# Optimization experiments

Measured on AMD Instinct MI355X. Metric: run time of the kernel, lower is better.

## Reference

```python
import jax, jax.numpy as jnp
import numpy as np

EPS = 0.0001
N_NODES = 8192
N_GRAPHS = 128
NODES_PER_G = 64
N_FEAT = 128
CLDIM = 512
LAYERS = 3
HEADS = 8
HID = 64
N_EDGES = 262144
N_CLASSES = 10


def setup_inputs():
    key = jax.random.key(0)
    ks = jax.random.split(key, 12)
    x = jax.random.normal(ks[0], (N_NODES, N_FEAT), jnp.float32)

    def rand_edges(k):
        k1, k2 = jax.random.split(k)
        g = jax.random.randint(k1, (N_EDGES,), 0, N_GRAPHS)
        loc = jax.random.randint(k2, (2, N_EDGES), 0, NODES_PER_G)
        return (g[None, :] * NODES_PER_G + loc).astype(jnp.int32)

    edge_index = rand_edges(ks[1])
    neg_edge_index = rand_edges(ks[2])
    batch = (jnp.arange(N_NODES) // NODES_PER_G).astype(jnp.int32)
    # mask indices: all within-graph node pairs (block-diagonal mask==1)
    base = jnp.arange(N_GRAPHS) * NODES_PER_G
    a = jnp.repeat(jnp.arange(NODES_PER_G), NODES_PER_G)
    b = jnp.tile(jnp.arange(NODES_PER_G), NODES_PER_G)
    midx = jnp.stack([
        (base[:, None] + a[None, :]).reshape(-1),
        (base[:, None] + b[None, :]).reshape(-1),
    ]).astype(jnp.int32)
    s = 0.05
    return dict(
        x=x, edge_index=edge_index, neg_edge_index=neg_edge_index,
        batch=batch, midx=midx,
        fc_W=jax.random.normal(ks[3], (N_FEAT, CLDIM), jnp.float32) * s,
        fc_b=jnp.zeros((CLDIM,), jnp.float32),
        bn_g=jnp.ones((LAYERS, CLDIM), jnp.float32),
        bn_b=jnp.zeros((LAYERS, CLDIM), jnp.float32),
        conv_W=jax.random.normal(ks[4], (LAYERS, CLDIM, CLDIM), jnp.float32) * s,
        conv_b=jnp.zeros((LAYERS, CLDIM), jnp.float32),
        feat_W=jax.random.normal(ks[5], (LAYERS * CLDIM, HEADS * HID), jnp.float32) * s,
        phi=jax.random.normal(ks[6], (HEADS, 2 * HID, 1), jnp.float32) * s,
        fc1_W=jax.random.normal(ks[7], (HEADS * HID, HID), jnp.float32) * s,
        fc1_b=jnp.zeros((HID,), jnp.float32),
        fc2_W=jax.random.normal(ks[8], (HID, N_CLASSES), jnp.float32) * s,
        fc2_b=jnp.zeros((N_CLASSES,), jnp.float32),
    )


def _bn(h, g, b):
    # BatchNorm1d in training mode (biased variance over nodes)
    m = jnp.mean(h, 0)
    v = jnp.var(h, 0)
    return (h - m) * jax.lax.rsqrt(v + 1e-5) * g + b


def _gcn(h, W, b, src, dst, n):
    # GCNConv with added self-loops: D^-1/2 (A+I) D^-1/2 (h W) + b
    h2 = h @ W
    deg = jax.ops.segment_sum(jnp.ones(src.shape[0], h.dtype), dst, n) + 1.0
    dinv = jax.lax.rsqrt(deg)
    coef = (dinv[src] * dinv[dst])[:, None]
    agg = jax.ops.segment_sum(h2[src] * coef, dst, n)
    return agg + h2 / deg[:, None] + b


def _forward(x, fc_W, fc_b, bn_g, bn_b, conv_W, conv_b, feat_W, phi,
             fc1_W, fc1_b, fc2_W, fc2_b, edge_index, neg_edge_index, batch, midx):
    n = x.shape[0]
    h = x @ fc_W + fc_b
    src, dst = edge_index[0], edge_index[1]
    hs = []
    for i in range(LAYERS):
        h = _bn(h, bn_g[i], bn_b[i])
        h = jax.nn.relu(_gcn(h, conv_W[i], conv_b[i], src, dst, n))
        hs.append(h)
    z = jnp.concatenate(hs, -1)  # [N, LAYERS*CLDIM]

    # ---- recon loss: per-edge inner-product decoder, mean-pooled per graph ----
    def edge_loss(ei, neg):
        v = jnp.sum(z[ei[0]] * z[ei[1]], -1)
        sgm = jax.nn.sigmoid(v)
        l = -jnp.log(EPS + (1.0 - sgm if neg else sgm))
        seg = batch[ei[0]]
        cnt = jax.ops.segment_sum(jnp.ones_like(l), seg, N_GRAPHS)
        tot = jax.ops.segment_sum(l, seg, N_GRAPHS)
        return jnp.sum(tot / jnp.maximum(cnt, 1.0))

    Lrc = (edge_loss(edge_index, False) + edge_loss(neg_edge_index, True)) / N_GRAPHS

    # ---- classifier: multi-head sigmoid attention over mask pairs ----
    xh = (z @ feat_W).reshape(n, HEADS, HID)
    phi_a = phi[:, :HID, 0]   # [H, HID]
    phi_b = phi[:, HID:, 0]   # [H, HID]
    # cat([x_i, x_j]) @ phi == x_i @ phi_a + x_j @ phi_b, computed per node then gathered
    s1 = jnp.einsum('nhd,hd->nh', xh, phi_a)
    s2 = jnp.einsum('nhd,hd->nh', xh, phi_b)
    w = jax.nn.sigmoid(jax.nn.leaky_relu(s1[midx[0]] + s2[midx[1]]))  # [M, H]
    msg = (xh[midx[1]] * w[:, :, None]).reshape(-1, HEADS * HID)      # [M, H*HID]
    agg = jax.ops.segment_sum(msg, midx[0], n)
    logits = jax.nn.leaky_relu(agg @ fc1_W + fc1_b) @ fc2_W + fc2_b
    tmp = jnp.exp(logits - jnp.max(logits, -1, keepdims=True)) + EPS
    preds = tmp / jnp.sum(tmp, -1, keepdims=True)
    cnt = jax.ops.segment_sum(jnp.ones((n,), preds.dtype), batch, N_GRAPHS)
    yp = jax.ops.segment_sum(preds, batch, N_GRAPHS) / cnt[:, None]
    return jnp.log(yp), Lrc, preds


def reference(x, edge_index, neg_edge_index, batch, midx, fc_W, fc_b, bn_g, bn_b,
              conv_W, conv_b, feat_W, phi, fc1_W, fc1_b, fc2_W, fc2_b):
    return _forward(x, fc_W, fc_b, bn_g, bn_b, conv_W, conv_b, feat_W, phi,
                    fc1_W, fc1_b, fc2_W, fc2_b, edge_index, neg_edge_index, batch, midx)
```

## Files before the change

### kernel.cpp

```cpp
#include <hip/hip_runtime.h>

#define NN 8192
#define NG 128
#define NF 128
#define CL 512
#define ZD 1536
#define NE 262144

typedef __attribute__((ext_vector_type(8))) _Float16 half8;
typedef __attribute__((ext_vector_type(4))) float f32x4;

__global__ void deg_kernel(const int* __restrict__ dst, float* __restrict__ deg) {
    int e = blockIdx.x * 256 + threadIdx.x;
    atomicAdd(&deg[dst[e]], 1.0f);
}

__global__ void build_adj(const int* __restrict__ src, const int* __restrict__ dst,
                          const float* __restrict__ deg, float* __restrict__ A) {
    int e = blockIdx.x * 256 + threadIdx.x;
    int s = src[e], d = dst[e];
    int g = d >> 6;
    float w = rsqrtf(deg[s] + 1.0f) * rsqrtf(deg[d] + 1.0f);
    atomicAdd(&A[(size_t)((g << 6) + (d & 63)) * 64 + (s & 63)], w);
}

__global__ void cvtA(const float* __restrict__ Amat, const float* __restrict__ deg,
                     _Float16* __restrict__ Ah) {
    int t = blockIdx.x * 256 + threadIdx.x;
    int i4 = t * 4;
    int g = i4 >> 12, loc = i4 & 4095;
    float4 v = *(const float4*)(Amat + (size_t)g * 4096 + loc);
    float vv[4] = {v.x, v.y, v.z, v.w};
    int row = loc >> 6;
    int c0 = loc & 63;
    int ed = row - c0;
    if (ed >= 0 && ed < 4) vv[ed] += 1.0f / (deg[g * 64 + row] + 1.0f);
    int swz = (row & 7) << 3;
    #pragma unroll
    for (int e = 0; e < 4; ++e)
        Ah[(size_t)g * 4096 + ((loc + e) ^ swz)] = (_Float16)vv[e];
}

__global__ void cvt_h(const float* __restrict__ in, _Float16* __restrict__ out) {
    int i = blockIdx.x * 256 + threadIdx.x;
    float4 a = *(const float4*)(in + (size_t)i * 8);
    float4 b = *(const float4*)(in + (size_t)i * 8 + 4);
    half8 o;
    o[0] = (_Float16)a.x; o[1] = (_Float16)a.y; o[2] = (_Float16)a.z; o[3] = (_Float16)a.w;
    o[4] = (_Float16)b.x; o[5] = (_Float16)b.y; o[6] = (_Float16)b.z; o[7] = (_Float16)b.w;
    *(half8*)(out + (size_t)i * 8) = o;
}

__global__ void cvtT(const float* __restrict__ W, _Float16* __restrict__ Wt,
                     int Kd, int Nd) {
    __shared__ float t[32][33];
    int kb = blockIdx.y * 32, nb = blockIdx.x * 32;
    int tx = threadIdx.x, ty = threadIdx.y;
    for (int i = ty; i < 32; i += 8)
        t[i][tx] = W[(size_t)(kb + i) * Nd + nb + tx];
    __syncthreads();
    for (int i = ty; i < 32; i += 8)
        Wt[(size_t)(nb + i) * Kd + kb + tx] = (_Float16)t[tx][i];
}

__global__ void wprep(const float* __restrict__ W,
                      const float* __restrict__ sums, const float* __restrict__ sqs,
                      const float* __restrict__ g, const float* __restrict__ b,
                      _Float16* __restrict__ Wt, float* __restrict__ bias2,
                      int Kd, int Nd) {
    __shared__ float t[32][33];
    __shared__ float tks[32];
    int kb = blockIdx.y * 32, nb = blockIdx.x * 32;
    int tx = threadIdx.x, ty = threadIdx.y;
    for (int i = ty; i < 32; i += 8)
        t[i][tx] = W[(size_t)(kb + i) * Nd + nb + tx];
    int kc = kb + tx;
    float m = sums[kc] * (1.0f / NN);
    float var = sqs[kc] * (1.0f / NN) - m * m;
    float sc = rsqrtf(var + 1e-5f) * g[kc];
    if (ty == 0) tks[tx] = b[kc] - m * sc;
    __syncthreads();
    for (int i = ty; i < 32; i += 8)
        Wt[(size_t)(nb + i) * Kd + kb + tx] = (_Float16)(t[tx][i] * sc);
    if (ty == 0) {
        float acc = 0.f;
        #pragma unroll
        for (int i = 0; i < 32; ++i) acc = fmaf(tks[i], t[i][tx], acc);
        atomicAdd(&bias2[nb + tx], acc);
    }
}

template<int ACT, bool HASB, bool OUT16, bool STATS, bool FUSE>
__global__ __launch_bounds__(256)
void gemm_f16(const _Float16* __restrict__ A, int lda,
              const _Float16* __restrict__ Bt, int ldb,
              float* __restrict__ Cf, _Float16* __restrict__ Ch, int ldc,
              const float* __restrict__ bias, int K,
              float* __restrict__ sums, float* __restrict__ sqs,
              const _Float16* __restrict__ Ahg,
              const float* __restrict__ cb,
              _Float16* __restrict__ Zout)
{
    __shared__ __align__(16) char SMraw[FUSE ? 34816 : 24576];
    _Float16* As = (_Float16*)SMraw;
    _Float16* Bs = (_Float16*)(SMraw + 16384);
    const int tid = threadIdx.x;
    const int lane = tid & 63, wave = tid >> 6;
    const int wr = wave >> 1, wc = wave & 1;
    const int ntile = gridDim.x;
    const int li = blockIdx.y * ntile + blockIdx.x;
    const int x8 = li & 7, rest = li >> 3;
    const int bt = rest % ntile;
    const int bp = (rest / ntile) * 8 + x8;
    const int bm = bp * 128, bn = bt * 64;

    f32x4 acc[4][2];
    #pragma unroll
    for (int m = 0; m < 4; ++m)
        #pragma unroll
        for (int n = 0; n < 2; ++n)
            acc[m][n] = (f32x4){0.f, 0.f, 0.f, 0.f};

    const int fl = lane & 15, kh = (lane >> 4) * 8;
    const int sw = (fl & 7) << 3;

    for (int k0 = 0; k0 < K; k0 += 64) {
        #pragma unroll
        for (int j = 0; j < 4; ++j) {
            int d = wave * 2048 + j * 512 + lane * 8;
            int row = d >> 6, kk = d & 63;
            int sk = kk ^ ((row & 7) << 3);
            __builtin_amdgcn_global_load_lds(
                (const __attribute__((address_space(1))) void*)(A + (size_t)(bm + row) * lda + k0 + sk),
                (__attribute__((address_space(3))) void*)&As[wave * 2048 + j * 512], 16, 0, 0);
        }
        #pragma unroll
        for (int j = 0; j < 2; ++j) {
            int d = wave * 1024 + j * 512 + lane * 8;
            int row = d >> 6, kk = d & 63;
            int sk = kk ^ ((row & 7) << 3);
            __builtin_amdgcn_global_load_lds(
                (const __attribute__((address_space(1))) void*)(Bt + (size_t)(bn + row) * ldb + k0 + sk),
                (__attribute__((address_space(3))) void*)&Bs[wave * 1024 + j * 512], 16, 0, 0);
        }
        __syncthreads();
        #pragma unroll
        for (int kc = 0; kc < 2; ++kc) {
            int ko = (kc * 32 + kh) ^ sw;
            half8 av[4], bv[2];
            #pragma unroll
            for (int m = 0; m < 4; ++m)
                av[m] = *(const half8*)&As[(wr * 64 + m * 16 + fl) * 64 + ko];
            #pragma unroll
            for (int n = 0; n < 2; ++n)
                bv[n] = *(const half8*)&Bs[(wc * 32 + n * 16 + fl) * 64 + ko];
            #pragma unroll
            for (int m = 0; m < 4; ++m)
                #pragma unroll
                for (int n = 0; n < 2; ++n)
                    acc[m][n] = __builtin_amdgcn_mfma_f32_16x16x32_f16(av[m], bv[n], acc[m][n], 0, 0, 0);
        }
        __syncthreads();
    }

    const int orow0 = (lane >> 4) * 4;
    const int ocol  = lane & 15;

    if constexpr (!FUSE) {
        #pragma unroll
        for (int n = 0; n < 2; ++n) {
            int col = bn + wc * 32 + n * 16 + ocol;
            float bb = HASB ? bias[col] : 0.f;
            float ss = 0.f, qq = 0.f;
            #pragma unroll
            for (int m = 0; m < 4; ++m) {
                #pragma unroll
                for (int r = 0; r < 4; ++r) {
                    int rowg = bm + wr * 64 + m * 16 + orow0 + r;
                    float v = acc[m][n][r] + bb;
                    if (ACT == 2) v = v > 0.f ? v : 0.01f * v;
                    if (STATS) { ss += v; qq = fmaf(v, v, qq); }
                    if (OUT16) Ch[(size_t)rowg * ldc + col] = (_Float16)v;
                    else       Cf[(size_t)rowg * ldc + col] = v;
                }
            }
            if (STATS) {
                ss += __shfl_down(ss, 32); ss += __shfl_down(ss, 16);
                qq += __shfl_down(qq, 32); qq += __shfl_down(qq, 16);
                if (lane < 16) {
                    atomicAdd(&sums[col], ss);
                    atomicAdd(&sqs[col], qq);
                }
            }
        }
    } else {
        _Float16* AsA = (_Float16*)SMraw;
        _Float16* Xs  = (_Float16*)(SMraw + 16384);
        const _Float16* Ag = Ahg + (size_t)(bm >> 6) * 4096;
        #pragma unroll
        for (int j = 0; j < 4; ++j)
            __builtin_amdgcn_global_load_lds(
                (const __attribute__((address_space(1))) void*)(Ag + wave * 2048 + j * 512 + lane * 8),
                (__attribute__((address_space(3))) void*)&AsA[wave * 2048 + j * 512], 16, 0, 0);
        #pragma unroll
        for (int n = 0; n < 2; ++n) {
            int c = wc * 32 + n * 16 + ocol;
            float bb = HASB ? bias[bn + c] : 0.f;
            int csw = (c & 7) << 3;
            #pragma unroll
            for (int m = 0; m < 4; ++m) {
                #pragma unroll
                for (int r = 0; r < 4; ++r) {
                    int srow = wr * 64 + m * 16 + orow0 + r;
                    Xs[c * 128 + (srow & 64) + ((srow & 63) ^ csw)] = (_Float16)(acc[m][n][r] + bb);
                }
            }
        }
        __syncthreads();
        const int gg = wave >> 1, rh = wave & 1;
        f32x4 acc2[2][4];
        #pragma unroll
        for (int m2 = 0; m2 < 2; ++m2)
            #pragma unroll
            for (int n2 = 0; n2 < 4; ++n2)
                acc2[m2][n2] = (f32x4){0.f, 0.f, 0.f, 0.f};
        #pragma unroll
        for (int kc = 0; kc < 2; ++kc) {
            int ko = (kc * 32 + kh) ^ sw;
            #pragma unroll
            for (int m2 = 0; m2 < 2; ++m2) {
                int arow = rh * 32 + m2 * 16 + fl;
                half8 av = *(const half8*)&AsA[gg * 4096 + arow * 64 + ko];
                #pragma unroll
                for (int n2 = 0; n2 < 4; ++n2) {
                    int c = n2 * 16 + fl;
                    half8 bv = *(const half8*)&Xs[c * 128 + gg * 64 + ((kc * 32 + kh) ^ ((c & 7) << 3))];
                    acc2[m2][n2] = __builtin_amdgcn_mfma_f32_16x16x32_f16(av, bv, acc2[m2][n2], 0, 0, 0);
                }
            }
        }
        __syncthreads();
        float* Cs = (float*)SMraw;
        #pragma unroll
        for (int m2 = 0; m2 < 2; ++m2)
            #pragma unroll
            for (int n2 = 0; n2 < 4; ++n2)
                #pragma unroll
                for (int r = 0; r < 4; ++r)
                    Cs[(gg * 64 + rh * 32 + m2 * 16 + orow0 + r) * 68 + n2 * 16 + ocol] = acc2[m2][n2][r];
        __syncthreads();
        const int rr = tid >> 3, dq = tid & 7;
        #pragma unroll
        for (int pass = 0; pass < 4; ++pass) {
            int row = pass * 32 + rr;
            half8 hv;
            #pragma unroll
            for (int e = 0; e < 8; ++e) {
                float v = Cs[row * 68 + dq * 8 + e] + cb[bn + dq * 8 + e];
                v = v > 0.f ? v : 0.f;
                hv[e] = (_Float16)v;
            }
            *(half8*)(Zout + (size_t)(bm + row) * ZD + bn + dq * 8) = hv;
        }
        if (STATS && tid < 64) {
            float bb = cb[bn + tid];
            float ss = 0.f, qq = 0.f;
            for (int row = 0; row < 128; ++row) {
                float v = Cs[row * 68 + tid] + bb;
                v = v > 0.f ? v : 0.f;
                ss += v;
                qq = fmaf(v, v, qq);
            }
            atomicAdd(&sums[bn + tid], ss);
            atomicAdd(&sqs[bn + tid], qq);
        }
    }
}

__global__ __launch_bounds__(256)
void gram_mfma(const _Float16* __restrict__ Z, float* __restrict__ Gparts)
{
    __shared__ _Float16 Zs[4096];
    const int g = blockIdx.x, khalf = blockIdx.y;
    const int tid = threadIdx.x;
    const int lane = tid & 63, wave = tid >> 6;
    const int fl = lane & 15, kh = (lane >> 4) * 8;
    const int sw = (fl & 7) << 3;
    float* G = Gparts + (size_t)khalf * NG * 4096;

    f32x4 acc[4];
    #pragma unroll
    for (int n = 0; n < 4; ++n) acc[n] = (f32x4){0.f, 0.f, 0.f, 0.f};

    for (int k0 = khalf * (ZD / 2); k0 < (khalf + 1) * (ZD / 2); k0 += 64) {
        #pragma unroll
        for (int j = 0; j < 2; ++j) {
            int d = wave * 1024 + j * 512 + lane * 8;
            int row = d >> 6, kk = d & 63;
            int sk = kk ^ ((row & 7) << 3);
            __builtin_amdgcn_global_load_lds(
                (const __attribute__((address_space(1))) void*)(Z + (size_t)(g * 64 + row) * ZD + k0 + sk),
                (__attribute__((address_space(3))) void*)&Zs[wave * 1024 + j * 512], 16, 0, 0);
        }
        __syncthreads();
        #pragma unroll
        for (int kc = 0; kc < 2; ++kc) {
            int ko = (kc * 32 + kh) ^ sw;
            half8 av = *(const half8*)&Zs[(wave * 16 + fl) * 64 + ko];
            #pragma unroll
            for (int n = 0; n < 4; ++n) {
                half8 bv = *(const half8*)&Zs[(n * 16 + fl) * 64 + ko];
                acc[n] = __builtin_amdgcn_mfma_f32_16x16x32_f16(av, bv, acc[n], 0, 0, 0);
            }
        }
        __syncthreads();
    }
    const int orow0 = (lane >> 4) * 4;
    const int ocol  = lane & 15;
    #pragma unroll
    for (int n = 0; n < 4; ++n)
        #pragma unroll
        for (int r = 0; r < 4; ++r)
            G[(size_t)(g * 64 + wave * 16 + orow0 + r) * 64 + n * 16 + ocol] = acc[n][r];
}

__global__ void edge_loss2(const int* __restrict__ ei, const int* __restrict__ nei,
                           const float* __restrict__ G0, float* __restrict__ LOSS)
{
    const int setid = blockIdx.y;
    const int* e0 = setid ? nei : ei;
    const int* e1 = e0 + NE;
    float* tot = LOSS + setid * 256;
    float* cnt = tot + 128;
    const float* G1 = G0 + (size_t)NG * 4096;
    __shared__ float lt[128];
    __shared__ float lc[128];
    int tid = threadIdx.x;
    if (tid < 128) { lt[tid] = 0.f; lc[tid] = 0.f; }
    __syncthreads();
    for (int e = blockIdx.x * blockDim.x + tid; e < NE; e += gridDim.x * blockDim.x) {
        int a = e0[e], b = e1[e];
        int g = a >> 6;
        size_t idx = (size_t)((g << 6) + (a & 63)) * 64 + (b & 63);
        float v = G0[idx] + G1[idx];
        float s = 1.f / (1.f + expf(-v));
        float p = setid ? (1.f - s) : s;
        float l = -logf(1e-4f + p);
        atomicAdd(&lt[g], l);
        atomicAdd(&lc[g], 1.f);
    }
    __syncthreads();
    if (tid < 128) {
        atomicAdd(&tot[tid], lt[tid]);
        atomicAdd(&cnt[tid], lc[tid]);
    }
}

__global__ void lrc_final(const float* __restrict__ loss, float* __restrict__ out)
{
    int t = threadIdx.x;
    float v = loss[t] / fmaxf(loss[128 + t], 1.f) + loss[256 + t] / fmaxf(loss[384 + t], 1.f);
    __shared__ float red[128];
    red[t] = v;
    __syncthreads();
    for (int s = 64; s; s >>= 1) {
        if (t < s) red[t] += red[t + s];
        __syncthreads();
    }
    if (t == 0) out[0] = red[0] * (1.0f / 128.0f);
}

__global__ __launch_bounds__(256)
void featattn(const _Float16* __restrict__ Z, const _Float16* __restrict__ featWt,
              const float* __restrict__ phi, _Float16* __restrict__ agg)
{
    __shared__ __align__(16) char SMraw[34816];
    _Float16* As = (_Float16*)SMraw;
    _Float16* Bs = (_Float16*)(SMraw + 8192);
    float*    Cs = (float*)SMraw;
    _Float16* Xt = (_Float16*)(SMraw + 17408);
    _Float16* Ws = (_Float16*)(SMraw + 25600);
    float*    s1s = (float*)(SMraw + 33792);
    float*    s2s = (float*)(SMraw + 34048);
    const int h = blockIdx.x, g = blockIdx.y;
    const int tid = threadIdx.x;
    const int lane = tid & 63, wave = tid >> 6;
    const int fl = lane & 15, kh = (lane >> 4) * 8;
    const int sw = (fl & 7) << 3;

    f32x4 acc[4];
    #pragma unroll
    for (int n = 0; n < 4; ++n) acc[n] = (f32x4){0.f, 0.f, 0.f, 0.f};

    for (int k0 = 0; k0 < ZD; k0 += 64) {
        #pragma unroll
        for (int j = 0; j < 2; ++j) {
            int d = wave * 1024 + j * 512 + lane * 8;
            int row = d >> 6, kk = d & 63;
            int sk = kk ^ ((row & 7) << 3);
            __builtin_amdgcn_global_load_lds(
                (const __attribute__((address_space(1))) void*)(Z + (size_t)(g * 64 + row) * ZD + k0 + sk),
                (__attribute__((address_space(3))) void*)&As[wave * 1024 + j * 512], 16, 0, 0);
            __builtin_amdgcn_global_load_lds(
                (const __attribute__((address_space(1))) void*)(featWt + (size_t)(h * 64 + row) * ZD + k0 + sk),
                (__attribute__((address_space(3))) void*)&Bs[wave * 1024 + j * 512], 16, 0, 0);
        }
        __syncthreads();
        #pragma unroll
        for (int kc = 0; kc < 2; ++kc) {
            int ko = (kc * 32 + kh) ^ sw;
            half8 av = *(const half8*)&As[(wave * 16 + fl) * 64 + ko];
            #pragma unroll
            for (int n = 0; n < 4; ++n) {
                half8 bv = *(const half8*)&Bs[(n * 16 + fl) * 64 + ko];
                acc[n] = __builtin_amdgcn_mfma_f32_16x16x32_f16(av, bv, acc[n], 0, 0, 0);
            }
        }
        __syncthreads();
    }
    const int orow0 = (lane >> 4) * 4, ocol = lane & 15;
    #pragma unroll
    for (int n = 0; n < 4; ++n)
        #pragma unroll
        for (int r = 0; r < 4; ++r)
            Cs[(wave * 16 + orow0 + r) * 68 + n * 16 + ocol] = acc[n][r];
    __syncthreads();
    {
        const int b = tid >> 2, dq = tid & 3;
        const float* pa = phi + h * 128 + dq * 16;
        const float* pb = pa + 64;
        float sa = 0.f, sb = 0.f;
        #pragma unroll
        for (int j = 0; j < 16; ++j) {
            int d = dq * 16 + j;
            float vf = Cs[b * 68 + d];
            Xt[(d * 64 + b) ^ ((d & 7) << 3)] = (_Float16)vf;
            sa = fmaf(vf, pa[j], sa);
            sb = fmaf(vf, pb[j], sb);
        }
        sa += __shfl_down(sa, 2); sa += __shfl_down(sa, 1);
        sb += __shfl_down(sb, 2); sb += __shfl_down(sb, 1);
        if (dq == 0) { s1s[b] = sa; s2s[b] = sb; }
    }
    __syncthreads();
    {
        const int i = tid >> 2, bq = tid & 3;
        float si = s1s[i];
        #pragma unroll
        for (int e = 0; e < 16; ++e) {
            int b = bq * 16 + e;
            float t = si + s2s[b];
            t = t > 0.f ? t : 0.01f * t;
            float w = 1.f / (1.f + expf(-t));
            Ws[(i * 64 + b) ^ ((i & 7) << 3)] = (_Float16)w;
        }
    }
    __syncthreads();
    f32x4 acc2[4];
    #pragma unroll
    for (int n = 0; n < 4; ++n) acc2[n] = (f32x4){0.f, 0.f, 0.f, 0.f};
    #pragma unroll
    for (int kc = 0; kc < 2; ++kc) {
        int rowa = wave * 16 + fl;
        half8 av = *(const half8*)&Ws[(rowa * 64 + kc * 32 + kh) ^ ((rowa & 7) << 3)];
        #pragma unroll
        for (int n = 0; n < 4; ++n) {
            int rowb = n * 16 + fl;
            half8 bv = *(const half8*)&Xt[(rowb * 64 + kc * 32 + kh) ^ ((rowb & 7) << 3)];
            acc2[n] = __builtin_amdgcn_mfma_f32_16x16x32_f16(av, bv, acc2[n], 0, 0, 0);
        }
    }
    __syncthreads();
    #pragma unroll
    for (int n = 0; n < 4; ++n)
        #pragma unroll
        for (int r = 0; r < 4; ++r)
            Cs[(wave * 16 + orow0 + r) * 68 + n * 16 + ocol] = acc2[n][r];
    __syncthreads();
    {
        const int rr = tid >> 3, dq = tid & 7;
        #pragma unroll
        for (int half = 0; half < 2; ++half) {
            int nd = half * 32 + rr;
            half8 hv;
            #pragma unroll
            for (int e = 0; e < 8; ++e)
                hv[e] = (_Float16)Cs[nd * 68 + dq * 8 + e];
            *(half8*)(agg + (size_t)(g * 64 + nd) * CL + h * 64 + dq * 8) = hv;
        }
    }
}

__global__ __launch_bounds__(256)
void fc1head(const _Float16* __restrict__ AGG, const _Float16* __restrict__ fc1Wt,
             const float* __restrict__ fc1b,
             const float* __restrict__ fc2W, const float* __restrict__ fc2b,
             float* __restrict__ preds, float* __restrict__ outlog)
{
    __shared__ __align__(16) char SMraw[17664];
    _Float16* As = (_Float16*)SMraw;
    _Float16* Bs = (_Float16*)(SMraw + 8192);
    float*    Cs = (float*)SMraw;
    const int g = blockIdx.x;
    const int tid = threadIdx.x;
    const int lane = tid & 63, wave = tid >> 6;
    const int fl = lane & 15, kh = (lane >> 4) * 8;
    const int sw = (fl & 7) << 3;

    f32x4 acc[4];
    #pragma unroll
    for (int n = 0; n < 4; ++n) acc[n] = (f32x4){0.f, 0.f, 0.f, 0.f};

    for (int k0 = 0; k0 < CL; k0 += 64) {
        #pragma unroll
        for (int j = 0; j < 2; ++j) {
            int d = wave * 1024 + j * 512 + lane * 8;
            int row = d >> 6, kk = d & 63;
            int sk = kk ^ ((row & 7) << 3);
            __builtin_amdgcn_global_load_lds(
                (const __attribute__((address_space(1))) void*)(AGG + (size_t)(g * 64 + row) * CL + k0 + sk),
                (__attribute__((address_space(3))) void*)&As[wave * 1024 + j * 512], 16, 0, 0);
            __builtin_amdgcn_global_load_lds(
                (const __attribute__((address_space(1))) void*)(fc1Wt + (size_t)row * CL + k0 + sk),
                (__attribute__((address_space(3))) void*)&Bs[wave * 1024 + j * 512], 16, 0, 0);
        }
        __syncthreads();
        #pragma unroll
        for (int kc = 0; kc < 2; ++kc) {
            int ko = (kc * 32 + kh) ^ sw;
            half8 av = *(const half8*)&As[(wave * 16 + fl) * 64 + ko];
            #pragma unroll
            for (int n = 0; n < 4; ++n) {
                half8 bv = *(const half8*)&Bs[(n * 16 + fl) * 64 + ko];
                acc[n] = __builtin_amdgcn_mfma_f32_16x16x32_f16(av, bv, acc[n], 0, 0, 0);
            }
        }
        __syncthreads();
    }
    const int orow0 = (lane >> 4) * 4, ocol = lane & 15;
    #pragma unroll
    for (int n = 0; n < 4; ++n) {
        int col = n * 16 + ocol;
        float bb = fc1b[col];
        #pragma unroll
        for (int r = 0; r < 4; ++r) {
            float v = acc[n][r] + bb;
            v = v > 0.f ? v : 0.01f * v;
            Cs[(wave * 16 + orow0 + r) * 69 + col] = v;
        }
    }
    __syncthreads();
    if (tid < 64) {
        float lg[10];
        float mx = -1e30f;
        #pragma unroll
        for (int c = 0; c < 10; ++c) {
            float s = fc2b[c];
            #pragma unroll
            for (int k = 0; k < 64; ++k) s = fmaf(Cs[tid * 69 + k], fc2W[k * 10 + c], s);
            lg[c] = s;
            mx = fmaxf(mx, s);
        }
        float sum = 0.f;
        #pragma unroll
        for (int c = 0; c < 10; ++c) {
            float t = expf(lg[c] - mx) + 1e-4f;
            lg[c] = t;
            sum += t;
        }
        float inv = 1.f / sum;
        #pragma unroll
        for (int c = 0; c < 10; ++c) {
            lg[c] *= inv;
            preds[(size_t)(g * 64 + tid) * 10 + c] = lg[c];
        }
        #pragma unroll
        for (int off = 32; off; off >>= 1)
            #pragma unroll
            for (int c = 0; c < 10; ++c) lg[c] += __shfl_down(lg[c], off);
        if (tid == 0)
            #pragma unroll
            for (int c = 0; c < 10; ++c) outlog[g * 10 + c] = logf(lg[c] * (1.0f / 64.0f));
    }
}

extern "C" void kernel_launch(void* const* d_in, const int* in_sizes, int n_in,
                              void* d_out, int out_size, void* d_ws, size_t ws_size,
                              hipStream_t stream)
{
    (void)in_sizes; (void)n_in; (void)out_size; (void)ws_size;
    const float* x     = (const float*)d_in[0];
    const int*   ei    = (const int*)d_in[1];
    const int*   nei   = (const int*)d_in[2];
    const float* fcW   = (const float*)d_in[5];
    const float* fcb   = (const float*)d_in[6];
    const float* bng   = (const float*)d_in[7];
    const float* bnb   = (const float*)d_in[8];
    const float* convW = (const float*)d_in[9];
    const float* convb = (const float*)d_in[10];
    const float* featW = (const float*)d_in[11];
    const float* phi   = (const float*)d_in[12];
    const float* fc1W  = (const float*)d_in[13];
    const float* fc1b  = (const float*)d_in[14];
    const float* fc2W  = (const float*)d_in[15];
    const float* fc2b  = (const float*)d_in[16];
    float* out = (float*)d_out;

    char* ws = (char*)d_ws;
    _Float16* Z       = (_Float16*)(ws);
    _Float16* H0      = (_Float16*)(ws + 25165824);
    _Float16* AGG     = (_Float16*)(ws + 33554432);
    _Float16* xb      = (_Float16*)(ws + 41943040);
    _Float16* fcWt    = (_Float16*)(ws + 44040192);
    _Float16* convWs  = (_Float16*)(ws + 44171264);
    _Float16* featWt  = (_Float16*)(ws + 44695552);
    _Float16* fc1Wt   = (_Float16*)(ws + 46268416);
    _Float16* Ah      = (_Float16*)(ws + 46333952);
    float*    Gram    = (float*)(ws + 47382528);
    float*    DEG     = (float*)(ws + 51576832);
    float*    Amat    = (float*)(ws + 51609600);
    float*    LOSS    = (float*)(ws + 53706752);
    float*    BNS3    = (float*)(ws + 53708800);
    float*    B2      = (float*)(ws + 53721088);

    const int* src = ei;
    const int* dst = ei + NE;

    hipMemsetAsync(DEG, 0, 53727232 - 51576832, stream);

    deg_kernel<<<NE / 256, 256, 0, stream>>>(dst, DEG);
    build_adj<<<NE / 256, 256, 0, stream>>>(src, dst, DEG, Amat);
    cvtA<<<(NG * 4096 / 4) / 256, 256, 0, stream>>>(Amat, DEG, Ah);

    cvt_h<<<(NN * NF / 8) / 256, 256, 0, stream>>>(x, xb);
    cvtT<<<dim3(CL / 32, NF / 32), dim3(32, 8), 0, stream>>>(fcW, fcWt, NF, CL);
    cvtT<<<dim3(CL / 32, ZD / 32), dim3(32, 8), 0, stream>>>(featW, featWt, ZD, CL);
    cvtT<<<dim3(2, 16), dim3(32, 8), 0, stream>>>(fc1W, fc1Wt, 512, 64);

    gemm_f16<0, true, true, true, false><<<dim3(CL / 64, NN / 128), 256, 0, stream>>>(
        xb, NF, fcWt, NF, nullptr, H0, CL, fcb, NF, BNS3, BNS3 + 512,
        nullptr, nullptr, nullptr);

    for (int i = 0; i < 3; ++i) {
        const _Float16* Ain = (i == 0) ? H0 : (Z + (size_t)(i - 1) * CL);
        int lda = (i == 0) ? CL : ZD;
        float* sums = BNS3 + i * 1024;
        float* sqs  = sums + 512;
        float* b2   = B2 + i * 512;
        wprep<<<dim3(CL / 32, CL / 32), dim3(32, 8), 0, stream>>>(
            convW + (size_t)i * CL * CL, sums, sqs, bng + i * CL, bnb + i * CL,
            convWs, b2, CL, CL);
        if (i < 2)
            gemm_f16<0, true, false, true, true><<<dim3(CL / 64, NN / 128), 256, 0, stream>>>(
                Ain, lda, convWs, CL, nullptr, nullptr, 0, b2, CL,
                BNS3 + (i + 1) * 1024, BNS3 + (i + 1) * 1024 + 512,
                Ah, convb + i * CL, Z + (size_t)i * CL);
        else
            gemm_f16<0, true, false, false, true><<<dim3(CL / 64, NN / 128), 256, 0, stream>>>(
                Ain, lda, convWs, CL, nullptr, nullptr, 0, b2, CL,
                nullptr, nullptr, Ah, convb + i * CL, Z + (size_t)i * CL);
    }

    gram_mfma<<<dim3(NG, 2), 256, 0, stream>>>(Z, Gram);
    edge_loss2<<<dim3(128, 2), 256, 0, stream>>>(ei, nei, Gram, LOSS);
    lrc_final<<<1, 128, 0, stream>>>(LOSS, out + 1280);

    featattn<<<dim3(8, NG), 256, 0, stream>>>(Z, featWt, phi, AGG);

    fc1head<<<NG, 256, 0, stream>>>(AGG, fc1Wt, fc1b, fc2W, fc2b, out + 1281, out);
}
```

Measured before the change: 187.6 us.

## Tile featattn over two graphs per block with 2x2 wave layout

Each featattn block now handles 128 nodes (two graphs) for one head instead of 64 nodes, using a 2x2 wave arrangement where each wave computes a 64x32 output tile with 4x2 MFMA accumulators. This raises MFMA work per LDS load and halves how often the featW tile is reloaded per node, and the grid changes from 8x128 to 64x8. The attention stage is reorganised to run per graph within the block. The cost is double the LDS footprint (about 67KB), which lowers occupancy, and half as many blocks.

```diff
diff --git a/kernel.cpp b/kernel.cpp
--- a/kernel.cpp
+++ b/kernel.cpp
@@ -374,34 +374,45 @@
 void featattn(const _Float16* __restrict__ Z, const _Float16* __restrict__ featWt,
               const float* __restrict__ phi, _Float16* __restrict__ agg)
 {
-    __shared__ __align__(16) char SMraw[34816];
-    _Float16* As = (_Float16*)SMraw;
-    _Float16* Bs = (_Float16*)(SMraw + 8192);
-    float*    Cs = (float*)SMraw;
-    _Float16* Xt = (_Float16*)(SMraw + 17408);
-    _Float16* Ws = (_Float16*)(SMraw + 25600);
-    float*    s1s = (float*)(SMraw + 33792);
-    float*    s2s = (float*)(SMraw + 34048);
-    const int h = blockIdx.x, g = blockIdx.y;
+    __shared__ __align__(16) char SMraw[68608];
+    _Float16* As  = (_Float16*)SMraw;
+    _Float16* Bs  = (_Float16*)(SMraw + 16384);
+    float*    Cs  = (float*)SMraw;
+    _Float16* Xt  = (_Float16*)(SMraw + 34816);
+    _Float16* Ws  = (_Float16*)(SMraw + 51200);
+    float*    s1s = (float*)(SMraw + 67584);
+    float*    s2s = (float*)(SMraw + 68096);
+    const int pnl = blockIdx.x, h = blockIdx.y;
+    const int bm = pnl * 128;
     const int tid = threadIdx.x;
     const int lane = tid & 63, wave = tid >> 6;
+    const int wr = wave >> 1, wc = wave & 1;
     const int fl = lane & 15, kh = (lane >> 4) * 8;
     const int sw = (fl & 7) << 3;
 
-    f32x4 acc[4];
-    #pragma unroll
-    for (int n = 0; n < 4; ++n) acc[n] = (f32x4){0.f, 0.f, 0.f, 0.f};
+    f32x4 acc[4][2];
+    #pragma unroll
+    for (int m = 0; m < 4; ++m)
+        #pragma unroll
+        for (int n = 0; n < 2; ++n)
+            acc[m][n] = (f32x4){0.f, 0.f, 0.f, 0.f};
 
     for (int k0 = 0; k0 < ZD; k0 += 64) {
+        #pragma unroll
+        for (int j = 0; j < 4; ++j) {
+            int d = wave * 2048 + j * 512 + lane * 8;
+            int row = d >> 6, kk = d & 63;
+            int sk = kk ^ ((row & 7) << 3);
+            __builtin_amdgcn_global_load_lds(
+                (const __attribute__((address_space(1))) void*)(Z + (size_t)(bm + row) * ZD + k0 + sk),
+                (__attribute__((address_space(3))) void*)&As[wave * 2048 + j * 512], 16, 0, 0);
+        }
         #pragma unroll
         for (int j = 0; j < 2; ++j) {
             int d = wave * 1024 + j * 512 + lane * 8;
             int row = d >> 6, kk = d & 63;
             int sk = kk ^ ((row & 7) << 3);
             __builtin_amdgcn_global_load_lds(
-                (const __attribute__((address_space(1))) void*)(Z + (size_t)(g * 64 + row) * ZD + k0 + sk),
-                (__attribute__((address_space(3))) void*)&As[wave * 1024 + j * 512], 16, 0, 0);
-            __builtin_amdgcn_global_load_lds(
                 (const __attribute__((address_space(1))) void*)(featWt + (size_t)(h * 64 + row) * ZD + k0 + sk),
                 (__attribute__((address_space(3))) void*)&Bs[wave * 1024 + j * 512], 16, 0, 0);
         }
@@ -409,84 +420,105 @@
         #pragma unroll
         for (int kc = 0; kc < 2; ++kc) {
             int ko = (kc * 32 + kh) ^ sw;
-            half8 av = *(const half8*)&As[(wave * 16 + fl) * 64 + ko];
-            #pragma unroll
-            for (int n = 0; n < 4; ++n) {
-                half8 bv = *(const half8*)&Bs[(n * 16 + fl) * 64 + ko];
-                acc[n] = __builtin_amdgcn_mfma_f32_16x16x32_f16(av, bv, acc[n], 0, 0, 0);
-            }
+            half8 av[4], bv[2];
+            #pragma unroll
+            for (int m = 0; m < 4; ++m)
+                av[m] = *(const half8*)&As[(wr * 64 + m * 16 + fl) * 64 + ko];
+            #pragma unroll
+            for (int n = 0; n < 2; ++n)
+                bv[n] = *(const half8*)&Bs[(wc * 32 + n * 16 + fl) * 64 + ko];
+            #pragma unroll
+            for (int m = 0; m < 4; ++m)
+                #pragma unroll
+                for (int n = 0; n < 2; ++n)
+                    acc[m][n] = __builtin_amdgcn_mfma_f32_16x16x32_f16(av[m], bv[n], acc[m][n], 0, 0, 0);
         }
         __syncthreads();
     }
     const int orow0 = (lane >> 4) * 4, ocol = lane & 15;
     #pragma unroll
-    for (int n = 0; n < 4; ++n)
-        #pragma unroll
-        for (int r = 0; r < 4; ++r)
-            Cs[(wave * 16 + orow0 + r) * 68 + n * 16 + ocol] = acc[n][r];
+    for (int n = 0; n < 2; ++n) {
+        int col = wc * 32 + n * 16 + ocol;
+        #pragma unroll
+        for (int m = 0; m < 4; ++m)
+            #pragma unroll
+            for (int r = 0; r < 4; ++r)
+                Cs[(wr * 64 + m * 16 + orow0 + r) * 68 + col] = acc[m][n][r];
+    }
     __syncthreads();
     {
-        const int b = tid >> 2, dq = tid & 3;
-        const float* pa = phi + h * 128 + dq * 16;
+        const int bnode = tid >> 1, dq = tid & 1;
+        const int gg = bnode >> 6, bloc = bnode & 63;
+        const float* pa = phi + h * 128 + dq * 32;
         const float* pb = pa + 64;
         float sa = 0.f, sb = 0.f;
         #pragma unroll
-        for (int j = 0; j < 16; ++j) {
-            int d = dq * 16 + j;
-            float vf = Cs[b * 68 + d];
-            Xt[(d * 64 + b) ^ ((d & 7) << 3)] = (_Float16)vf;
+        for (int j = 0; j < 32; ++j) {
+            int d = dq * 32 + j;
+            float vf = Cs[bnode * 68 + d];
+            Xt[gg * 4096 + ((d * 64 + bloc) ^ ((d & 7) << 3))] = (_Float16)vf;
             sa = fmaf(vf, pa[j], sa);
             sb = fmaf(vf, pb[j], sb);
         }
-        sa += __shfl_down(sa, 2); sa += __shfl_down(sa, 1);
-        sb += __shfl_down(sb, 2); sb += __shfl_down(sb, 1);
-        if (dq == 0) { s1s[b] = sa; s2s[b] = sb; }
+        sa += __shfl_down(sa, 1);
+        sb += __shfl_down(sb, 1);
+        if (dq == 0) { s1s[bnode] = sa; s2s[bnode] = sb; }
     }
     __syncthreads();
     {
-        const int i = tid >> 2, bq = tid & 3;
-        float si = s1s[i];
-        #pragma unroll
-        for (int e = 0; e < 16; ++e) {
-            int b = bq * 16 + e;
-            float t = si + s2s[b];
+        const int inode = tid >> 1, bq = tid & 1;
+        const int gg = inode >> 6, iloc = inode & 63;
+        float si = s1s[inode];
+        #pragma unroll
+        for (int e = 0; e < 32; ++e) {
+            int b = bq * 32 + e;
+            float t = si + s2s[gg * 64 + b];
             t = t > 0.f ? t : 0.01f * t;
             float w = 1.f / (1.f + expf(-t));
-            Ws[(i * 64 + b) ^ ((i & 7) << 3)] = (_Float16)w;
-        }
-    }
-    __syncthreads();
-    f32x4 acc2[4];
-    #pragma unroll
-    for (int n = 0; n < 4; ++n) acc2[n] = (f32x4){0.f, 0.f, 0.f, 0.f};
+            Ws[gg * 4096 + ((iloc * 64 + b) ^ ((iloc & 7) << 3))] = (_Float16)w;
+        }
+    }
+    __syncthreads();
+    const int gg = wave >> 1, rh = wave & 1;
+    f32x4 acc2[2][4];
+    #pragma unroll
+    for (int m2 = 0; m2 < 2; ++m2)
+        #pragma unroll
+        for (int n2 = 0; n2 < 4; ++n2)
+            acc2[m2][n2] = (f32x4){0.f, 0.f, 0.f, 0.f};
     #pragma unroll
     for (int kc = 0; kc < 2; ++kc) {
-        int rowa = wave * 16 + fl;
-        half8 av = *(const half8*)&Ws[(rowa * 64 + kc * 32 + kh) ^ ((rowa & 7) << 3)];
-        #pragma unroll
-        for (int n = 0; n < 4; ++n) {
-            int rowb = n * 16 + fl;
-            half8 bv = *(const half8*)&Xt[(rowb * 64 + kc * 32 + kh) ^ ((rowb & 7) << 3)];
-            acc2[n] = __builtin_amdgcn_mfma_f32_16x16x32_f16(av, bv, acc2[n], 0, 0, 0);
-        }
-    }
-    __syncthreads();
-    #pragma unroll
-    for (int n = 0; n < 4; ++n)
-        #pragma unroll
-        for (int r = 0; r < 4; ++r)
-            Cs[(wave * 16 + orow0 + r) * 68 + n * 16 + ocol] = acc2[n][r];
+        #pragma unroll
+        for (int m2 = 0; m2 < 2; ++m2) {
+            int arow = rh * 32 + m2 * 16 + fl;
+            half8 av = *(const half8*)&Ws[gg * 4096 + ((arow * 64 + kc * 32 + kh) ^ ((arow & 7) << 3))];
+            #pragma unroll
+            for (int n2 = 0; n2 < 4; ++n2) {
+                int rowb = n2 * 16 + fl;
+                half8 bv = *(const half8*)&Xt[gg * 4096 + ((rowb * 64 + kc * 32 + kh) ^ ((rowb & 7) << 3))];
+                acc2[m2][n2] = __builtin_amdgcn_mfma_f32_16x16x32_f16(av, bv, acc2[m2][n2], 0, 0, 0);
+            }
+        }
+    }
+    __syncthreads();
+    #pragma unroll
+    for (int m2 = 0; m2 < 2; ++m2)
+        #pragma unroll
+        for (int n2 = 0; n2 < 4; ++n2)
+            #pragma unroll
+            for (int r = 0; r < 4; ++r)
+                Cs[(gg * 64 + rh * 32 + m2 * 16 + orow0 + r) * 68 + n2 * 16 + ocol] = acc2[m2][n2][r];
     __syncthreads();
     {
         const int rr = tid >> 3, dq = tid & 7;
         #pragma unroll
-        for (int half = 0; half < 2; ++half) {
-            int nd = half * 32 + rr;
+        for (int pass = 0; pass < 4; ++pass) {
+            int row = pass * 32 + rr;
             half8 hv;
             #pragma unroll
             for (int e = 0; e < 8; ++e)
-                hv[e] = (_Float16)Cs[nd * 68 + dq * 8 + e];
-            *(half8*)(agg + (size_t)(g * 64 + nd) * CL + h * 64 + dq * 8) = hv;
+                hv[e] = (_Float16)Cs[row * 68 + dq * 8 + e];
+            *(half8*)(agg + (size_t)(bm + row) * CL + h * 64 + dq * 8) = hv;
         }
     }
 }
@@ -665,7 +697,7 @@
     edge_loss2<<<dim3(128, 2), 256, 0, stream>>>(ei, nei, Gram, LOSS);
     lrc_final<<<1, 128, 0, stream>>>(LOSS, out + 1280);
 
-    featattn<<<dim3(8, NG), 256, 0, stream>>>(Z, featWt, phi, AGG);
+    featattn<<<dim3(64, 8), 256, 0, stream>>>(Z, featWt, phi, AGG);
 
     fc1head<<<NG, 256, 0, stream>>>(AGG, fc1Wt, fc1b, fc2W, fc2b, out + 1281, out);
 }
```

New measurement: 177.8 us. 5.2% less time.
